# Optimization experiments

Hardware: AMD Instinct MI355X
Metric: run time of the kernel (lower is better)

Reference implementation:

```python
import jax, jax.numpy as jnp
import numpy as np

CS = 256
CT = 256
RED = 4


def _mlp(x, w1, b1, w2, b2):
    # Linear -> ReLU -> Linear -> Sigmoid (torch Linear: y = x @ W.T + b)
    h = jax.nn.relu(x @ w1.T + b1)
    return jax.nn.sigmoid(h @ w2.T + b2)


def _row_normalize(g, eps=1e-12):
    # F.normalize(g, p=2, dim=1)
    n = jnp.sqrt(jnp.sum(g * g, axis=1, keepdims=True))
    return g / jnp.maximum(n, eps)


def setup_inputs() -> dict:
    key = jax.random.key(0)
    ks = jax.random.split(key, 32)
    B, C, H, W = 128, 256, 28, 28
    inp = {
        'student': jax.random.normal(ks[0], (B, C, H, W), jnp.float32),
        'teacher': jax.random.normal(ks[1], (B, C, H, W), jnp.float32),
    }
    hid_cat = (CS + CT) // RED  # 128
    hid_s = CS // RED           # 64
    hid_t = CT // RED           # 64
    specs = [
        ('fc_s', CS + CT, hid_cat, CS),
        ('fc_s_add', CS, hid_s, CS),
        ('fc_s_mul', CS, hid_s, CS),
        ('fc_t', CS + CT, hid_cat, CT),
        ('fc_t_add', CT, hid_t, CT),
        ('fc_t_mul', CT, hid_t, CT),
    ]
    i = 2
    for name, din, dh, dout in specs:
        inp[name + '_w1'] = jax.random.normal(ks[i], (dh, din), jnp.float32) * 0.05
        inp[name + '_b1'] = jnp.zeros((dh,), jnp.float32)
        inp[name + '_w2'] = jax.random.normal(ks[i + 1], (dout, dh), jnp.float32) * 0.05
        inp[name + '_b2'] = jnp.zeros((dout,), jnp.float32)
        i += 2
    return inp


def reference(student, teacher,
              fc_s_w1, fc_s_b1, fc_s_w2, fc_s_b2,
              fc_s_add_w1, fc_s_add_b1, fc_s_add_w2, fc_s_add_b2,
              fc_s_mul_w1, fc_s_mul_b1, fc_s_mul_w2, fc_s_mul_b2,
              fc_t_w1, fc_t_b1, fc_t_w2, fc_t_b2,
              fc_t_add_w1, fc_t_add_b1, fc_t_add_w2, fc_t_add_b2,
              fc_t_mul_w1, fc_t_mul_b1, fc_t_mul_w2, fc_t_mul_b2):
    b_s, c_s = student.shape[0], student.shape[1]
    b_t, c_t = teacher.shape[0], teacher.shape[1]

    fm_s = student.reshape(b_s, -1)                 # [B, C*H*W]
    G_s = fm_s @ fm_s.T                             # [B, B]
    norm_G_s = _row_normalize(G_s)
    y_s = jnp.mean(student, axis=(2, 3))            # adaptive avg pool -> [B, C]

    fm_t = teacher.reshape(b_t, -1)
    G_t = fm_t @ fm_t.T
    norm_G_t = _row_normalize(G_t)
    y_t = jnp.mean(teacher, axis=(2, 3))

    zs = norm_G_s @ y_s                             # [B, c_s]
    zt = norm_G_t @ y_t                             # [B, c_t]
    z_add = zs + zt
    z_mul = zs * zt
    z = jnp.concatenate([zs, zt], axis=1)           # [B, c_s + c_t]

    g_s = _mlp(z, fc_s_w1, fc_s_b1, fc_s_w2, fc_s_b2)
    g_s_add = _mlp(z_add, fc_s_add_w1, fc_s_add_b1, fc_s_add_w2, fc_s_add_b2)
    g_s_mul = _mlp(z_mul, fc_s_mul_w1, fc_s_mul_b1, fc_s_mul_w2, fc_s_mul_b2)
    g_t = _mlp(z, fc_t_w1, fc_t_b1, fc_t_w2, fc_t_b2)
    g_t_add = _mlp(z_add, fc_t_add_w1, fc_t_add_b1, fc_t_add_w2, fc_t_add_b2)
    g_t_mul = _mlp(z_mul, fc_t_mul_w1, fc_t_mul_b1, fc_t_mul_w2, fc_t_mul_b2)

    # relu is a no-op after sigmoid but kept for faithfulness
    gate_s = (jax.nn.relu(g_s) + jax.nn.relu(g_s_add) + jax.nn.relu(g_s_mul))[:, :, None, None]
    gate_t = (jax.nn.relu(g_t) + jax.nn.relu(g_t_add) + jax.nn.relu(g_t_mul))[:, :, None, None]
    return gate_s * student, gate_t * teacher
```

## Files before the change

kernel.cpp:

```cpp
#include <hip/hip_runtime.h>


typedef __bf16 bf16x8 __attribute__((ext_vector_type(8)));
typedef float f32x4 __attribute__((ext_vector_type(4)));
typedef unsigned short ushortx8 __attribute__((ext_vector_type(8)));

#define LSTR 136

__device__ __forceinline__ unsigned short f2bf(float f) {
    unsigned int u = __float_as_uint(f);
    u += 0x7fffu + ((u >> 16) & 1u);
    return (unsigned short)(u >> 16);
}

__device__ __forceinline__ bf16x8 ldfrag(const unsigned short* p) {
    return __builtin_bit_cast(bf16x8, *reinterpret_cast<const ushortx8*>(p));
}

__global__ __launch_bounds__(256) void k_gram(
    const float* __restrict__ student, const float* __restrict__ teacher,
    float* __restrict__ partials,
    float* __restrict__ y_ws)
{
    const int blk = blockIdx.x;
    const int tensor = blk >> 8;
    const int ch = blk & 255;
    const float* __restrict__ src = tensor ? teacher : student;

    const int tid = threadIdx.x;
    const int wave = tid >> 6;
    const int lane = tid & 63;
    const int mrow = lane & 15;
    const int koff = (lane >> 4) * 8;

    __shared__ unsigned short lds[128 * LSTR];

    const int r = tid >> 1;
    const int half = tid & 1;

    {
        ushortx8 zz = {0, 0, 0, 0, 0, 0, 0, 0};
        *reinterpret_cast<ushortx8*>(&lds[r * LSTR + 112 + 8 * half]) = zz;
    }

    const float4* srow = reinterpret_cast<const float4*>(
        src + (size_t)r * 200704 + (size_t)ch * 784 + half * 56);
    unsigned short* dst = &lds[r * LSTR + half * 56];

    f32x4 acc[2][8];
    f32x4 zv = {0.f, 0.f, 0.f, 0.f};
#pragma unroll
    for (int a = 0; a < 2; ++a)
#pragma unroll
        for (int b = 0; b < 8; ++b) acc[a][b] = zv;

    float msum = 0.f;

    for (int t = 0; t < 7; ++t) {
        __syncthreads();
#pragma unroll
        for (int j = 0; j < 14; ++j) {
            float4 v = srow[t * 28 + j];
            msum += v.x + v.y + v.z + v.w;
            unsigned short h0 = f2bf(v.x), h1 = f2bf(v.y), h2 = f2bf(v.z), h3 = f2bf(v.w);
            unsigned long long packed =
                (unsigned long long)h0 | ((unsigned long long)h1 << 16) |
                ((unsigned long long)h2 << 32) | ((unsigned long long)h3 << 48);
            *reinterpret_cast<unsigned long long*>(dst + 4 * j) = packed;
        }
        __syncthreads();
#pragma unroll
        for (int kk = 0; kk < 4; ++kk) {
            const int col = kk * 32 + koff;
            bf16x8 a0 = ldfrag(&lds[(32 * wave + mrow) * LSTR + col]);
            bf16x8 a1 = ldfrag(&lds[(32 * wave + 16 + mrow) * LSTR + col]);
#pragma unroll
            for (int nt = 0; nt < 8; ++nt) {
                bf16x8 bb = ldfrag(&lds[(16 * nt + mrow) * LSTR + col]);
                acc[0][nt] = __builtin_amdgcn_mfma_f32_16x16x32_bf16(a0, bb, acc[0][nt], 0, 0, 0);
                acc[1][nt] = __builtin_amdgcn_mfma_f32_16x16x32_bf16(a1, bb, acc[1][nt], 0, 0, 0);
            }
        }
    }

    float other = __shfl_xor(msum, 1);
    if (half == 0)
        y_ws[tensor * 32768 + r * 256 + ch] = (msum + other) * (1.f / 784.f);

    float* pbase = partials + (size_t)blk * 16384;
    const int crow = (lane >> 4) * 4;
    const int ccol = lane & 15;
#pragma unroll
    for (int rt = 0; rt < 2; ++rt)
#pragma unroll
        for (int nt = 0; nt < 8; ++nt)
#pragma unroll
            for (int g = 0; g < 4; ++g) {
                int m = 32 * wave + 16 * rt + crow + g;
                int n = 16 * nt + ccol;
                pbase[m * 128 + n] = acc[rt][nt][g];
            }
}

__device__ __forceinline__ float sigm(float x) { return 1.f / (1.f + __expf(-x)); }

__device__ __forceinline__ float dotf4(const float* a, const float* __restrict__ b, int n4) {
    const float4* a4 = reinterpret_cast<const float4*>(a);
    const float4* b4 = reinterpret_cast<const float4*>(b);
    float s = 0.f;
    for (int d = 0; d < n4; ++d) {
        float4 x = a4[d], y = b4[d];
        s += x.x * y.x + x.y * y.y + x.z * y.z + x.w * y.w;
    }
    return s;
}

__global__ __launch_bounds__(256) void k_gates(
    const float* __restrict__ partials, const float* __restrict__ y_ws,
    float* __restrict__ gates,
    const float* __restrict__ fs_w1, const float* __restrict__ fs_b1,
    const float* __restrict__ fs_w2, const float* __restrict__ fs_b2,
    const float* __restrict__ fsa_w1, const float* __restrict__ fsa_b1,
    const float* __restrict__ fsa_w2, const float* __restrict__ fsa_b2,
    const float* __restrict__ fsm_w1, const float* __restrict__ fsm_b1,
    const float* __restrict__ fsm_w2, const float* __restrict__ fsm_b2,
    const float* __restrict__ ft_w1, const float* __restrict__ ft_b1,
    const float* __restrict__ ft_w2, const float* __restrict__ ft_b2,
    const float* __restrict__ fta_w1, const float* __restrict__ fta_b1,
    const float* __restrict__ fta_w2, const float* __restrict__ fta_b2,
    const float* __restrict__ ftm_w1, const float* __restrict__ ftm_b1,
    const float* __restrict__ ftm_w2, const float* __restrict__ ftm_b2)
{
    const int b = blockIdx.x;
    const int tid = threadIdx.x;
    const int wave = tid >> 6;
    const int lane = tid & 63;

    __shared__ __align__(16) float Gn[2][128];
    __shared__ float wred[4];
    __shared__ __align__(16) float z[512];
    __shared__ __align__(16) float za[256];
    __shared__ __align__(16) float zm[256];
    __shared__ __align__(16) float hbuf[256];
    __shared__ __align__(16) float h2buf[256];

    const int tt = tid >> 7;
    const int j = tid & 127;
    float g = 0.f;
    const float* pb = partials + (size_t)tt * 256 * 16384 + (size_t)b * 128 + j;
    for (int p = 0; p < 256; ++p) g += pb[(size_t)p * 16384];

    float v2 = g * g;
#pragma unroll
    for (int off = 32; off > 0; off >>= 1) v2 += __shfl_xor(v2, off);
    if (lane == 0) wred[wave] = v2;
    __syncthreads();
    float ss = tt ? (wred[2] + wred[3]) : (wred[0] + wred[1]);
    float inv = 1.f / fmaxf(sqrtf(ss), 1e-12f);
    Gn[tt][j] = g * inv;
    __syncthreads();

    const int c = tid;
    float zs = 0.f, zt = 0.f;
    const float* ys = y_ws;
    const float* yt = y_ws + 32768;
    for (int jj = 0; jj < 128; ++jj) {
        zs = fmaf(Gn[0][jj], ys[jj * 256 + c], zs);
        zt = fmaf(Gn[1][jj], yt[jj * 256 + c], zt);
    }
    z[c] = zs;
    z[256 + c] = zt;
    za[c] = zs + zt;
    zm[c] = zs * zt;
    __syncthreads();

    {
        const int h = tid & 127;
        const float* w = (tid < 128) ? (fs_w1 + h * 512) : (ft_w1 + h * 512);
        const float* bb = (tid < 128) ? fs_b1 : ft_b1;
        hbuf[tid] = fmaxf(bb[h] + dotf4(z, w, 128), 0.f);
    }
    {
        const int q = tid >> 6;
        const int i = tid & 63;
        const float* w = (q == 0) ? fsa_w1 : (q == 1) ? fta_w1 : (q == 2) ? fsm_w1 : ftm_w1;
        const float* bb = (q == 0) ? fsa_b1 : (q == 1) ? fta_b1 : (q == 2) ? fsm_b1 : ftm_b1;
        const float* in = (q < 2) ? za : zm;
        h2buf[tid] = fmaxf(bb[i] + dotf4(in, w + i * 256, 64), 0.f);
    }
    __syncthreads();

    {
        float gs  = sigm(fs_b2[c]  + dotf4(hbuf,        fs_w2  + c * 128, 32));
        float gt  = sigm(ft_b2[c]  + dotf4(hbuf + 128,  ft_w2  + c * 128, 32));
        float gsa = sigm(fsa_b2[c] + dotf4(h2buf,       fsa_w2 + c * 64, 16));
        float gta = sigm(fta_b2[c] + dotf4(h2buf + 64,  fta_w2 + c * 64, 16));
        float gsm = sigm(fsm_b2[c] + dotf4(h2buf + 128, fsm_w2 + c * 64, 16));
        float gtm = sigm(ftm_b2[c] + dotf4(h2buf + 192, ftm_w2 + c * 64, 16));
        gates[b * 256 + c] = gs + gsa + gsm;
        gates[32768 + b * 256 + c] = gt + gta + gtm;
    }
}

__global__ __launch_bounds__(256) void k_apply(
    const float4* __restrict__ student4, const float4* __restrict__ teacher4,
    const float* __restrict__ gates, float4* __restrict__ out4)
{
    const unsigned i = blockIdx.x * 256u + threadIdx.x;
    const unsigned PER = 6422528u;
    const unsigned isT = (i >= PER) ? 1u : 0u;
    const unsigned jj = i - isT * PER;
    const unsigned bc = jj / 196u;
    const float g = gates[isT * 32768u + bc];
    const float4* in = isT ? teacher4 : student4;
    float4 v = in[jj];
    v.x *= g; v.y *= g; v.z *= g; v.w *= g;
    out4[i] = v;
}

extern "C" void kernel_launch(void* const* d_in, const int* in_sizes, int n_in,
                              void* d_out, int out_size, void* d_ws, size_t ws_size,
                              hipStream_t stream) {
    (void)in_sizes; (void)n_in; (void)out_size; (void)ws_size;

    const float* student = (const float*)d_in[0];
    const float* teacher = (const float*)d_in[1];
    const float* fs_w1  = (const float*)d_in[2];
    const float* fs_b1  = (const float*)d_in[3];
    const float* fs_w2  = (const float*)d_in[4];
    const float* fs_b2  = (const float*)d_in[5];
    const float* fsa_w1 = (const float*)d_in[6];
    const float* fsa_b1 = (const float*)d_in[7];
    const float* fsa_w2 = (const float*)d_in[8];
    const float* fsa_b2 = (const float*)d_in[9];
    const float* fsm_w1 = (const float*)d_in[10];
    const float* fsm_b1 = (const float*)d_in[11];
    const float* fsm_w2 = (const float*)d_in[12];
    const float* fsm_b2 = (const float*)d_in[13];
    const float* ft_w1  = (const float*)d_in[14];
    const float* ft_b1  = (const float*)d_in[15];
    const float* ft_w2  = (const float*)d_in[16];
    const float* ft_b2  = (const float*)d_in[17];
    const float* fta_w1 = (const float*)d_in[18];
    const float* fta_b1 = (const float*)d_in[19];
    const float* fta_w2 = (const float*)d_in[20];
    const float* fta_b2 = (const float*)d_in[21];
    const float* ftm_w1 = (const float*)d_in[22];
    const float* ftm_b1 = (const float*)d_in[23];
    const float* ftm_w2 = (const float*)d_in[24];
    const float* ftm_b2 = (const float*)d_in[25];

    float* out = (float*)d_out;
    float* partials = out;
    float* y_ws = (float*)d_ws;
    float* gates = y_ws + 65536;

    k_gram<<<dim3(512), dim3(256), 0, stream>>>(student, teacher, partials, y_ws);
    k_gates<<<dim3(128), dim3(256), 0, stream>>>(partials, y_ws, gates,
        fs_w1, fs_b1, fs_w2, fs_b2,
        fsa_w1, fsa_b1, fsa_w2, fsa_b2,
        fsm_w1, fsm_b1, fsm_w2, fsm_b2,
        ft_w1, ft_b1, ft_w2, ft_b2,
        fta_w1, fta_b1, fta_w2, fta_b2,
        ftm_w1, ftm_b1, ftm_w2, ftm_b2);
    k_apply<<<dim3(50176), dim3(256), 0, stream>>>(
        (const float4*)student, (const float4*)teacher, gates, (float4*)out);
}
```

Before: 488.5 us.

## Prefetch gram tiles into registers, transpose partials layout, add nontemporal output stores

The gram kernel now loads the next K-slice into registers while MFMAs run on the current LDS tile, and uses hardware bf16 conversion instead of manual rounding. It also adds a two-block occupancy hint. Partials are stored transposed so each gates block reads contiguous float4 rows, with the reduction split across all 256 threads instead of 256 strided scalar loads. The apply kernel uses nontemporal stores. The costs are higher register pressure from the 14-float4 prefetch buffer, and a possibly different bf16 rounding path.

```diff
diff --git a/kernel.cpp b/kernel.cpp
--- a/kernel.cpp
+++ b/kernel.cpp
@@ -2,22 +2,17 @@
 
 
 typedef __bf16 bf16x8 __attribute__((ext_vector_type(8)));
+typedef __bf16 bf16x4 __attribute__((ext_vector_type(4)));
 typedef float f32x4 __attribute__((ext_vector_type(4)));
 typedef unsigned short ushortx8 __attribute__((ext_vector_type(8)));
 
 #define LSTR 136
 
-__device__ __forceinline__ unsigned short f2bf(float f) {
-    unsigned int u = __float_as_uint(f);
-    u += 0x7fffu + ((u >> 16) & 1u);
-    return (unsigned short)(u >> 16);
-}
-
 __device__ __forceinline__ bf16x8 ldfrag(const unsigned short* p) {
     return __builtin_bit_cast(bf16x8, *reinterpret_cast<const ushortx8*>(p));
 }
 
-__global__ __launch_bounds__(256) void k_gram(
+__global__ __launch_bounds__(256, 2) void k_gram(
     const float* __restrict__ student, const float* __restrict__ teacher,
     float* __restrict__ partials,
     float* __restrict__ y_ws)
@@ -56,19 +51,25 @@
 
     float msum = 0.f;
 
+    float4 v[14];
+#pragma unroll
+    for (int j = 0; j < 14; ++j) v[j] = srow[j];
+
     for (int t = 0; t < 7; ++t) {
+#pragma unroll
+        for (int j = 0; j < 14; ++j) {
+            float4 w = v[j];
+            msum += (w.x + w.y) + (w.z + w.w);
+            bf16x4 hv = {(__bf16)w.x, (__bf16)w.y, (__bf16)w.z, (__bf16)w.w};
+            *reinterpret_cast<bf16x4*>(dst + 4 * j) = hv;
+        }
         __syncthreads();
-#pragma unroll
-        for (int j = 0; j < 14; ++j) {
-            float4 v = srow[t * 28 + j];
-            msum += v.x + v.y + v.z + v.w;
-            unsigned short h0 = f2bf(v.x), h1 = f2bf(v.y), h2 = f2bf(v.z), h3 = f2bf(v.w);
-            unsigned long long packed =
-                (unsigned long long)h0 | ((unsigned long long)h1 << 16) |
-                ((unsigned long long)h2 << 32) | ((unsigned long long)h3 << 48);
-            *reinterpret_cast<unsigned long long*>(dst + 4 * j) = packed;
-        }
-        __syncthreads();
+
+        if (t < 6) {
+#pragma unroll
+            for (int j = 0; j < 14; ++j) v[j] = srow[(t + 1) * 28 + j];
+        }
+
 #pragma unroll
         for (int kk = 0; kk < 4; ++kk) {
             const int col = kk * 32 + koff;
@@ -81,15 +82,16 @@
                 acc[1][nt] = __builtin_amdgcn_mfma_f32_16x16x32_bf16(a1, bb, acc[1][nt], 0, 0, 0);
             }
         }
+        __syncthreads();
     }
 
     float other = __shfl_xor(msum, 1);
     if (half == 0)
         y_ws[tensor * 32768 + r * 256 + ch] = (msum + other) * (1.f / 784.f);
 
-    float* pbase = partials + (size_t)blk * 16384;
     const int crow = (lane >> 4) * 4;
     const int ccol = lane & 15;
+    const size_t blkoff = (size_t)blk * 128;
 #pragma unroll
     for (int rt = 0; rt < 2; ++rt)
 #pragma unroll
@@ -98,7 +100,7 @@
             for (int g = 0; g < 4; ++g) {
                 int m = 32 * wave + 16 * rt + crow + g;
                 int n = 16 * nt + ccol;
-                pbase[m * 128 + n] = acc[rt][nt][g];
+                partials[((size_t)m << 16) + blkoff + n] = acc[rt][nt][g];
             }
 }
 
@@ -143,12 +145,27 @@
     __shared__ __align__(16) float zm[256];
     __shared__ __align__(16) float hbuf[256];
     __shared__ __align__(16) float h2buf[256];
+    __shared__ __align__(16) float red[8][128];
+
+    {
+        const int pg = tid >> 5;
+        const int jq = tid & 31;
+        const float4* pb4 = reinterpret_cast<const float4*>(partials + ((size_t)b << 16))
+                            + (size_t)(pg * 64) * 32 + jq;
+        float4 s = {0.f, 0.f, 0.f, 0.f};
+#pragma unroll 8
+        for (int p = 0; p < 64; ++p) {
+            float4 vv = pb4[p * 32];
+            s.x += vv.x; s.y += vv.y; s.z += vv.z; s.w += vv.w;
+        }
+        *reinterpret_cast<float4*>(&red[pg][jq * 4]) = s;
+    }
+    __syncthreads();
 
     const int tt = tid >> 7;
     const int j = tid & 127;
-    float g = 0.f;
-    const float* pb = partials + (size_t)tt * 256 * 16384 + (size_t)b * 128 + j;
-    for (int p = 0; p < 256; ++p) g += pb[(size_t)p * 16384];
+    float g = (red[tt * 4 + 0][j] + red[tt * 4 + 1][j]) +
+              (red[tt * 4 + 2][j] + red[tt * 4 + 3][j]);
 
     float v2 = g * g;
 #pragma unroll
@@ -204,7 +221,7 @@
 
 __global__ __launch_bounds__(256) void k_apply(
     const float4* __restrict__ student4, const float4* __restrict__ teacher4,
-    const float* __restrict__ gates, float4* __restrict__ out4)
+    const float* __restrict__ gates, float* __restrict__ out)
 {
     const unsigned i = blockIdx.x * 256u + threadIdx.x;
     const unsigned PER = 6422528u;
@@ -214,8 +231,8 @@
     const float g = gates[isT * 32768u + bc];
     const float4* in = isT ? teacher4 : student4;
     float4 v = in[jj];
-    v.x *= g; v.y *= g; v.z *= g; v.w *= g;
-    out4[i] = v;
+    f32x4 r = {v.x * g, v.y * g, v.z * g, v.w * g};
+    __builtin_nontemporal_store(r, reinterpret_cast<f32x4*>(out) + i);
 }
 
 extern "C" void kernel_launch(void* const* d_in, const int* in_sizes, int n_in,
@@ -264,5 +281,5 @@
         fta_w1, fta_b1, fta_w2, fta_b2,
         ftm_w1, ftm_b1, ftm_w2, ftm_b2);
     k_apply<<<dim3(50176), dim3(256), 0, stream>>>(
-        (const float4*)student, (const float4*)teacher, gates, (float4*)out);
-}
+        (const float4*)student, (const float4*)teacher, gates, out);
+}
```

Result: no change. 479.2 us (-1.9%).
